# Optimization experiments

Measured on AMD Instinct MI355X. Metric: run time of the kernel, lower is better.

The kernel has to match this reference:

```python
import jax, jax.numpy as jnp
import numpy as np

B, N, K = 8, 2048, 4          # graphs per batch, nodes per graph, knn k
IN_CH, HID, C = 16, 128, 64   # in_channels, GCN hidden, n_clusters
E = 262144                    # input edges


def gcn_conv(x, src, dst, W, b):
    """PyG GCNConv: self-loops + symmetric normalization + linear."""
    n = x.shape[0]
    xw = x @ W
    loop = jnp.arange(n)
    s2 = jnp.concatenate([src, loop])
    d2 = jnp.concatenate([dst, loop])
    deg = jax.ops.segment_sum(jnp.ones(s2.shape[0], x.dtype), d2, num_segments=n)
    dis = jax.lax.rsqrt(deg)  # deg >= 1 thanks to self loops
    norm = dis[s2] * dis[d2]
    return jax.ops.segment_sum(xw[s2] * norm[:, None], d2, num_segments=n) + b


def knn_edges(coords):
    """knn_graph(k=K, loop=False) per graph; edges neighbor->node (source_to_target)."""
    c = coords.reshape(B, N, 3)
    d2 = jnp.sum((c[:, :, None, :] - c[:, None, :, :]) ** 2, -1)  # [B,N,N]
    d2 = d2 + jnp.eye(N, dtype=c.dtype) * jnp.asarray(1e10, c.dtype)  # exclude self
    _, idx = jax.lax.top_k(-d2, K)  # [B,N,K] local neighbor indices
    offs = (jnp.arange(B) * N)[:, None, None]
    src = (idx + offs).reshape(-1)
    dst = (jnp.broadcast_to(jnp.arange(N)[None, :, None], (B, N, K)) + offs).reshape(-1)
    return src, dst


def dmon_pool(x, adj, Wp, bp):
    """PyG DMoNPooling (eval mode, mask all-true since graphs are equal-sized)."""
    s = jax.nn.softmax(x @ Wp + bp, axis=-1)              # [B,N,C]
    out = jax.nn.selu(jnp.einsum('bnc,bnf->bcf', s, x))   # [B,C,F]
    out_adj = jnp.einsum('bnc,bnm,bmd->bcd', s, adj, s)   # [B,C,C]
    deg = adj.sum(1)                                      # column sums, [B,N]
    m = deg.sum(-1) / 2                                   # [B]
    ca = jnp.einsum('bnc,bn->bc', s, deg)                 # [B,C]
    normalizer = ca[:, :, None] * ca[:, None, :] / (2 * m)[:, None, None]
    spectral = (-jnp.trace(out_adj - normalizer, axis1=1, axis2=2) / (2 * m)).mean()
    ss = jnp.einsum('bnc,bnd->bcd', s, s)
    ss_fro = jnp.linalg.norm(ss, axis=(1, 2), keepdims=True)
    i_norm = jnp.sqrt(jnp.asarray(C, x.dtype))            # ||I_C||_F
    i_s = jnp.eye(C, dtype=x.dtype)
    ortho = jnp.linalg.norm(ss / ss_fro - i_s / i_norm, axis=(1, 2)).mean()
    cluster = (jnp.linalg.norm(s.sum(1), axis=1) / N * i_norm - 1).mean()
    return s, out, spectral, ortho, cluster


def forward(x, edge_src, edge_dst, W1, b1, W2, b2, Wp, bp):
    h = jax.nn.relu(gcn_conv(x, edge_src, edge_dst, W1, b1))
    src2, dst2 = knn_edges(h[:, :3])                      # dynamic graph on dims [0,1,2]
    h = jax.nn.relu(gcn_conv(h, src2, dst2, W2, b2))
    xd = h.reshape(B, N, HID)                             # to_dense_batch (equal-size graphs)
    g = edge_src // N                                     # to_dense_adj on ORIGINAL edges
    adj = jnp.zeros((B, N, N), x.dtype).at[g, edge_src % N, edge_dst % N].add(1.0)
    s, out, sp, o, cl = dmon_pool(xd, adj, Wp, bp)
    return jax.nn.log_softmax(out, axis=-1), sp + o + cl, s


def setup_inputs():
    key = jax.random.key(0)
    ks = jax.random.split(key, 8)
    x = jax.random.normal(ks[0], (B * N, IN_CH), jnp.float32)
    g = jax.random.randint(ks[1], (E,), 0, B)
    edge_src = (g * N + jax.random.randint(ks[2], (E,), 0, N)).astype(jnp.int32)
    edge_dst = (g * N + jax.random.randint(ks[3], (E,), 0, N)).astype(jnp.int32)
    batch = jnp.repeat(jnp.arange(B, dtype=jnp.int32), N)
    W1 = jax.random.normal(ks[4], (IN_CH, HID), jnp.float32) / np.sqrt(IN_CH)
    b1 = jnp.zeros((HID,), jnp.float32)
    W2 = jax.random.normal(ks[5], (HID, HID), jnp.float32) / np.sqrt(HID)
    b2 = jnp.zeros((HID,), jnp.float32)
    Wp = jax.random.normal(ks[6], (HID, C), jnp.float32) / np.sqrt(HID)
    bp = jnp.zeros((C,), jnp.float32)
    return {"x": x, "edge_src": edge_src, "edge_dst": edge_dst, "batch": batch,
            "W1": W1, "b1": b1, "W2": W2, "b2": b2, "Wp": Wp, "bp": bp}


def reference(x, edge_src, edge_dst, batch, W1, b1, W2, b2, Wp, bp):
    del batch  # graphs are equal-sized contiguous blocks of N nodes
    return forward(x, edge_src, edge_dst, W1, b1, W2, b2, Wp, bp)
```

## Files before the change

kernel.cpp:

```cpp
#include <hip/hip_runtime.h>
#include <math.h>

#define BGR 8
#define NN 2048
#define KNN 4
#define INCH 16
#define HID 128
#define CL 64
#define NE 262144
#define NT (BGR*NN)

#define OFF_CNT   0
#define OFF_CSR   16384
#define OFF_H1    1064960
#define OFF_NBR   3162112
#define OFF_SS    3227648
#define OFF_H2    4276224
#define OFF_TR    6373376
#define OFF_CA    6373384
#define OFF_SSUM  6373896
#define OFF_MS    6374408
#define OFF_H1C   6374416

__global__ void k_init(int* cnt, float* small, float* loss) {
  int i = blockIdx.x * 256 + threadIdx.x;
  if (i < 16384) cnt[i] = 0;
  int j = i - 16384;
  if (j >= 0 && j < 1040) small[j] = 0.f;
  if (i == 0) loss[0] = 0.f;
}

__global__ void k_bucket(const int* __restrict__ src, const int* __restrict__ dst,
                         int* __restrict__ cnt, int* __restrict__ csr) {
  int e = blockIdx.x * 256 + threadIdx.x;
  if (e >= NE) return;
  int d = dst[e];
  int slot = atomicAdd(&cnt[d], 1);
  if (slot < 64) csr[(d << 6) + slot] = src[e];
}

__global__ __launch_bounds__(256) void k_gemm1(const int* __restrict__ cnt,
    const int* __restrict__ csr, const float* __restrict__ x,
    const float* __restrict__ W1, const float* __restrict__ b1,
    float* __restrict__ h1, float* __restrict__ h1c) {
  __shared__ float a1[16][17];
  __shared__ float w[INCH * HID];
  int tid = threadIdx.x;
  for (int i = tid; i < INCH * HID / 4; i += 256) ((float4*)w)[i] = ((const float4*)W1)[i];
  int nl = tid >> 4, ch = tid & 15;
  int n = blockIdx.x * 16 + nl;
  int cnRaw = cnt[n];
  int cn = cnRaw > 64 ? 64 : cnRaw;
  float dn = rsqrtf((float)cnRaw + 1.0f);
  const int* row = csr + (n << 6);
  float acc = 0.f;
  int sNext = (cn > 0) ? row[0] : 0;
  for (int e = 0; e < cn; e++) {
    int sc = sNext;
    if (e + 1 < cn) sNext = row[e + 1];
    float dis = rsqrtf((float)cnt[sc] + 1.0f);
    acc += x[sc * INCH + ch] * dis;
  }
  a1[nl][ch] = (acc + x[n * INCH + ch] * dn) * dn;
  __syncthreads();
  int j = tid & 127;
  int ng = (tid >> 7) * 8;
#pragma unroll
  for (int u = 0; u < 8; u++) {
    int node = ng + u;
    float s = b1[j];
#pragma unroll
    for (int c2 = 0; c2 < INCH; c2++) s += a1[node][c2] * w[c2 * HID + j];
    float v = fmaxf(s, 0.f);
    h1[(size_t)(blockIdx.x * 16 + node) * HID + j] = v;
    if (j < 4) h1c[(size_t)(blockIdx.x * 16 + node) * 4 + j] = v;
  }
}

__global__ __launch_bounds__(1024) void k_knn(const float* __restrict__ h1c, int* __restrict__ nbr) {
  __shared__ float4 c4[NN];
  int g = blockIdx.y, tid = threadIdx.x;
  const float4* src4 = (const float4*)h1c + (size_t)g * NN;
  for (int i = tid; i < NN; i += 1024) c4[i] = src4[i];
  __syncthreads();
  int wid = tid >> 6, lane = tid & 63;
  int row0 = blockIdx.x * 32 + wid * 2;
  float mx[2], my[2], mz[2];
#pragma unroll
  for (int r = 0; r < 2; r++) { float4 m = c4[row0 + r]; mx[r] = m.x; my[r] = m.y; mz[r] = m.z; }
  unsigned t0[2], t1[2], t2[2], t3[2];
#pragma unroll
  for (int r = 0; r < 2; r++) { t0[r] = t1[r] = t2[r] = t3[r] = 0xFFFFFFFFu; }
#pragma unroll 4
  for (int i = 0; i < 32; i++) {
    int j = i * 64 + lane;
    float4 p = c4[j];
#pragma unroll
    for (int r = 0; r < 2; r++) {
      float dx = p.x - mx[r], dy = p.y - my[r], dz = p.z - mz[r];
      float d2 = dx * dx + dy * dy + dz * dz;
      unsigned k = (__float_as_uint(d2) & 0xFFFFFFE0u) | (unsigned)i;
      if (j == row0 + r) k = 0xFFFFFFFFu;
      unsigned M0 = max(t0[r], k); t0[r] = min(t0[r], k);
      unsigned M1 = max(t1[r], M0); t1[r] = min(t1[r], M0);
      unsigned M2 = max(t2[r], M1); t2[r] = min(t2[r], M1);
      t3[r] = min(t3[r], M2);
    }
  }
#pragma unroll
  for (int r = 0; r < 2; r++) {
    unsigned a0 = t0[r], a1 = t1[r], a2 = t2[r], a3 = t3[r];
    int res[4];
#pragma unroll
    for (int k = 0; k < 4; k++) {
      int cj = (int)((a0 & 31u) << 6) | lane;
      unsigned wd = a0; int wj = cj;
#pragma unroll
      for (int off = 32; off; off >>= 1) {
        unsigned od = (unsigned)__shfl_xor((int)wd, off, 64);
        int oj = __shfl_xor(wj, off, 64);
        bool take = (od < wd) || (od == wd && oj < wj);
        wd = take ? od : wd; wj = take ? oj : wj;
      }
      res[k] = wj;
      bool pop = (cj == wj);
      a0 = pop ? a1 : a0; a1 = pop ? a2 : a1; a2 = pop ? a3 : a2;
      a3 = pop ? 0xFFFFFFFFu : a3;
    }
    if (lane == 0) {
      int node = g * NN + row0 + r;
      ((int4*)nbr)[node] = make_int4(g * NN + res[0], g * NN + res[1],
                                     g * NN + res[2], g * NN + res[3]);
    }
  }
}

__global__ __launch_bounds__(256) void k_gemm2s(const float* __restrict__ h1,
    const int* __restrict__ nbr, const float* __restrict__ W2,
    const float* __restrict__ b2, const float* __restrict__ Wp,
    const float* __restrict__ bp, float* __restrict__ h2,
    float* __restrict__ s_out) {
  __shared__ float smem[6144];
  float (*At)[33] = (float(*)[33])smem;
  float* Bt = smem + 1056;
  float (*H2t)[128] = (float(*)[128])smem;
  float* Wt = smem + 4096;
  int tid = threadIdx.x;
  int rbase = blockIdx.x * 32;
  int r = tid >> 3, q = tid & 7;
  int4 nb = ((const int4*)nbr)[rbase + r];
  const float4* h4 = (const float4*)h1;
  size_t r0 = (size_t)(rbase + r) * 32, rx = (size_t)nb.x * 32, ry = (size_t)nb.y * 32,
         rz = (size_t)nb.z * 32, rw = (size_t)nb.w * 32;
  int rg = tid >> 5;
  int cg = (tid & 31) * 4;
  float acc[4][4];
#pragma unroll
  for (int i = 0; i < 4; i++)
#pragma unroll
    for (int j = 0; j < 4; j++) acc[i][j] = 0.f;
  int kk = tid >> 5;
  int cc = (tid & 31) * 4;
  for (int k0 = 0; k0 < HID; k0 += 32) {
    {
      int q4 = (k0 >> 2) + q;
      float4 a = h4[r0 + q4], bx = h4[rx + q4], by = h4[ry + q4],
             bz = h4[rz + q4], bw = h4[rw + q4];
      int k = q * 4;
      At[r][k]     = (a.x + bx.x + by.x + bz.x + bw.x) * 0.2f;
      At[r][k + 1] = (a.y + bx.y + by.y + bz.y + bw.y) * 0.2f;
      At[r][k + 2] = (a.z + bx.z + by.z + bz.z + bw.z) * 0.2f;
      At[r][k + 3] = (a.w + bx.w + by.w + bz.w + bw.w) * 0.2f;
    }
#pragma unroll
    for (int u = 0; u < 4; u++)
      *(float4*)&Bt[(kk + u * 8) * 128 + cc] = *(const float4*)&W2[(k0 + kk + u * 8) * HID + cc];
    __syncthreads();
#pragma unroll
    for (int k2 = 0; k2 < 32; k2++) {
      float4 bv = *(const float4*)&Bt[k2 * 128 + cg];
#pragma unroll
      for (int i = 0; i < 4; i++) {
        float av = At[rg * 4 + i][k2];
        acc[i][0] += av * bv.x; acc[i][1] += av * bv.y;
        acc[i][2] += av * bv.z; acc[i][3] += av * bv.w;
      }
    }
    __syncthreads();
  }
#pragma unroll
  for (int i = 0; i < 4; i++) {
    int rr = rbase + rg * 4 + i;
#pragma unroll
    for (int j = 0; j < 4; j++) {
      float v = acc[i][j] + b2[cg + j];
      v = fmaxf(v, 0.f);
      h2[(size_t)rr * HID + cg + j] = v;
      H2t[rg * 4 + i][cg + j] = v;
    }
  }
  int c0 = (tid & 31) * 2;
  float acc2[4][2];
  float bp0 = bp[c0], bp1 = bp[c0 + 1];
#pragma unroll
  for (int i = 0; i < 4; i++) { acc2[i][0] = bp0; acc2[i][1] = bp1; }
  for (int kt = 0; kt < 4; kt++) {
    *(float4*)&Wt[tid * 8]     = *(const float4*)&Wp[kt * 2048 + tid * 8];
    *(float4*)&Wt[tid * 8 + 4] = *(const float4*)&Wp[kt * 2048 + tid * 8 + 4];
    __syncthreads();
#pragma unroll
    for (int k2 = 0; k2 < 32; k2++) {
      float w0 = Wt[k2 * 64 + c0];
      float w1 = Wt[k2 * 64 + c0 + 1];
      int kg = kt * 32 + k2;
#pragma unroll
      for (int i = 0; i < 4; i++) {
        float av = H2t[rg * 4 + i][kg];
        acc2[i][0] += av * w0; acc2[i][1] += av * w1;
      }
    }
    __syncthreads();
  }
#pragma unroll
  for (int i = 0; i < 4; i++) {
    float m = fmaxf(acc2[i][0], acc2[i][1]);
    for (int off = 1; off < 32; off <<= 1) m = fmaxf(m, __shfl_xor(m, off, 64));
    float e0 = expf(acc2[i][0] - m), e1 = expf(acc2[i][1] - m);
    float sum = e0 + e1;
    for (int off = 1; off < 32; off <<= 1) sum += __shfl_xor(sum, off, 64);
    float inv = 1.0f / sum;
    size_t o = (size_t)(rbase + rg * 4 + i) * CL + c0;
    s_out[o] = e0 * inv;
    s_out[o + 1] = e1 * inv;
  }
}

__global__ __launch_bounds__(256) void k_dmon_trace(const float* __restrict__ s,
    const float* __restrict__ h2, const int* __restrict__ cnt,
    float* __restrict__ part_pool, float* __restrict__ part_ss,
    float* __restrict__ ca, float* __restrict__ ssum, float* __restrict__ msum,
    const int* __restrict__ src, const int* __restrict__ dst, float* __restrict__ tr) {
  __shared__ float st[64 * 64];
  __shared__ float ht[64 * 128];
  __shared__ float dt[64];
  __shared__ float red[256];
  __shared__ float bins[8];
  int tid = threadIdx.x;
  if (blockIdx.x < 256) {
    int b = blockIdx.x >> 5, sl = blockIdx.x & 31;
    int nb = sl * 64;
    const float* sp = s + ((size_t)b * NN + nb) * CL;
    const float* hp = h2 + ((size_t)b * NN + nb) * HID;
    for (int i = tid; i < 64 * 64 / 4; i += 256) ((float4*)st)[i] = ((const float4*)sp)[i];
    for (int i = tid; i < 64 * 128 / 4; i += 256) ((float4*)ht)[i] = ((const float4*)hp)[i];
    if (tid < 64) dt[tid] = (float)cnt[b * NN + nb + tid];
    __syncthreads();
    int tc = tid & 15, tf = tid >> 4;
    int c0 = tc * 4, f0 = tf * 8;
    float pacc[4][8];
#pragma unroll
    for (int i = 0; i < 4; i++)
#pragma unroll
      for (int j = 0; j < 8; j++) pacc[i][j] = 0.f;
    for (int n = 0; n < 64; n++) {
      float4 sv = *(const float4*)&st[n * 64 + c0];
      float4 ha = *(const float4*)&ht[n * 128 + f0];
      float4 hb = *(const float4*)&ht[n * 128 + f0 + 4];
      float svv[4] = {sv.x, sv.y, sv.z, sv.w};
#pragma unroll
      for (int i = 0; i < 4; i++) {
        pacc[i][0] += svv[i] * ha.x; pacc[i][1] += svv[i] * ha.y;
        pacc[i][2] += svv[i] * ha.z; pacc[i][3] += svv[i] * ha.w;
        pacc[i][4] += svv[i] * hb.x; pacc[i][5] += svv[i] * hb.y;
        pacc[i][6] += svv[i] * hb.z; pacc[i][7] += svv[i] * hb.w;
      }
    }
    float* pp = part_pool + ((size_t)(b * 32 + sl)) * 8192;
#pragma unroll
    for (int i = 0; i < 4; i++) {
      *(float4*)&pp[(c0 + i) * 128 + f0]     = make_float4(pacc[i][0], pacc[i][1], pacc[i][2], pacc[i][3]);
      *(float4*)&pp[(c0 + i) * 128 + f0 + 4] = make_float4(pacc[i][4], pacc[i][5], pacc[i][6], pacc[i][7]);
    }
    int d0 = tf * 4;
    float sacc[4][4];
#pragma unroll
    for (int i = 0; i < 4; i++)
#pragma unroll
      for (int j = 0; j < 4; j++) sacc[i][j] = 0.f;
    for (int n = 0; n < 64; n++) {
      float4 a = *(const float4*)&st[n * 64 + c0];
      float4 bq = *(const float4*)&st[n * 64 + d0];
      float av[4] = {a.x, a.y, a.z, a.w};
#pragma unroll
      for (int i = 0; i < 4; i++) {
        sacc[i][0] += av[i] * bq.x; sacc[i][1] += av[i] * bq.y;
        sacc[i][2] += av[i] * bq.z; sacc[i][3] += av[i] * bq.w;
      }
    }
    float* ps = part_ss + ((size_t)(b * 32 + sl)) * 4096;
#pragma unroll
    for (int i = 0; i < 4; i++)
      *(float4*)&ps[(c0 + i) * 64 + d0] = make_float4(sacc[i][0], sacc[i][1], sacc[i][2], sacc[i][3]);
    int c = tid & 63;
    int q = tid >> 6;
    float a_ss = 0, a_ca = 0, a_m = 0;
    for (int n = q; n < 64; n += 4) {
      float sv = st[n * 64 + c];
      float dv = dt[n];
      a_ss += sv; a_ca += sv * dv;
      if (c == 0) a_m += dv;
    }
    red[tid] = a_ss; __syncthreads();
    if (q == 0) atomicAdd(&ssum[b * CL + c], red[c] + red[64 + c] + red[128 + c] + red[192 + c]);
    __syncthreads();
    red[tid] = a_ca; __syncthreads();
    if (q == 0) atomicAdd(&ca[b * CL + c], red[c] + red[64 + c] + red[128 + c] + red[192 + c]);
    __syncthreads();
    red[tid] = (c == 0) ? a_m : 0.f; __syncthreads();
    if (tid == 0) atomicAdd(&msum[b], red[0] + red[64] + red[128] + red[192]);
  } else {
    if (tid < 8) bins[tid] = 0.f;
    __syncthreads();
    int sub = tid & 15;
    int grp = ((blockIdx.x - 256) * 256 + tid) >> 4;
    const float4* s4 = (const float4*)s;
    for (int e = grp; e < NE; e += 8192) {
      int se = src[e], de = dst[e];
      float4 a = s4[se * 16 + sub];
      float4 b = s4[de * 16 + sub];
      float v = a.x * b.x + a.y * b.y + a.z * b.z + a.w * b.w;
      v += __shfl_xor(v, 1, 64);
      v += __shfl_xor(v, 2, 64);
      v += __shfl_xor(v, 4, 64);
      v += __shfl_xor(v, 8, 64);
      if (sub == 0) atomicAdd(&bins[se >> 11], v);
    }
    __syncthreads();
    if (tid < 8) atomicAdd(&tr[tid], bins[tid]);
  }
}

__global__ __launch_bounds__(256) void k_final(const float* __restrict__ part_pool,
    const float* __restrict__ part_ss, const float* __restrict__ ca,
    const float* __restrict__ ssum, const float* __restrict__ msum,
    const float* __restrict__ tr, float* __restrict__ out, float* __restrict__ outs) {
  int tid = threadIdx.x;
  if (blockIdx.x < 256) {
    __shared__ float r[4], r2[4];
    int half = tid >> 7, f = tid & 127;
    int row = blockIdx.x * 2 + half;
    int wid = tid >> 6;
    const float* p = part_pool + (size_t)(row >> 6) * 32 * 8192 + (row & 63) * 128 + f;
    float v = 0.f;
#pragma unroll
    for (int sl = 0; sl < 32; sl++) v += p[sl * 8192];
    const float scale = 1.0507009873554805f, alpha = 1.6732632423543772f;
    v = scale * (v > 0.f ? v : alpha * expm1f(v));
    float m = v;
    for (int off = 32; off; off >>= 1) m = fmaxf(m, __shfl_xor(m, off, 64));
    if ((tid & 63) == 0) r[wid] = m;
    __syncthreads();
    m = fmaxf(r[half * 2], r[half * 2 + 1]);
    float e = expf(v - m);
    float sum = e;
    for (int off = 32; off; off >>= 1) sum += __shfl_xor(sum, off, 64);
    if ((tid & 63) == 0) r2[wid] = sum;
    __syncthreads();
    sum = r2[half * 2] + r2[half * 2 + 1];
    out[(size_t)row * HID + f] = v - m - logf(sum);
  } else {
    __shared__ float ssb[4096];
    __shared__ float red[256];
    int b = blockIdx.x - 256;
    float loc = 0.f;
    for (int idx = tid; idx < 4096; idx += 256) {
      const float* p = part_ss + (size_t)b * 32 * 4096 + idx;
      float v = 0.f;
#pragma unroll
      for (int sl = 0; sl < 32; sl++) v += p[sl * 4096];
      ssb[idx] = v;
      loc += v * v;
    }
    red[tid] = loc; __syncthreads();
    for (int s2 = 128; s2; s2 >>= 1) { if (tid < s2) red[tid] += red[tid + s2]; __syncthreads(); }
    float fro = sqrtf(red[0]);
    __syncthreads();
    loc = 0.f;
    for (int i = tid; i < 4096; i += 256) {
      float v = ssb[i] / fro - (((i % 65) == 0) ? 0.125f : 0.f);
      loc += v * v;
    }
    red[tid] = loc; __syncthreads();
    for (int s2 = 128; s2; s2 >>= 1) { if (tid < s2) red[tid] += red[tid + s2]; __syncthreads(); }
    float ortho_b = sqrtf(red[0]);
    __syncthreads();
    loc = 0.f;
    if (tid < 64) { float v = ca[b * 64 + tid]; loc = v * v; }
    red[tid] = loc; __syncthreads();
    for (int s2 = 128; s2; s2 >>= 1) { if (tid < s2) red[tid] += red[tid + s2]; __syncthreads(); }
    float caSq = red[0];
    __syncthreads();
    loc = 0.f;
    if (tid < 64) { float v = ssum[b * 64 + tid]; loc = v * v; }
    red[tid] = loc; __syncthreads();
    for (int s2 = 128; s2; s2 >>= 1) { if (tid < s2) red[tid] += red[tid + s2]; __syncthreads(); }
    float ssumSq = red[0];
    __syncthreads();
    if (tid == 0) {
      float m2 = msum[b];
      float spectral_b = -(tr[b] - caSq / m2) / m2;
      float cluster_b = sqrtf(ssumSq) / 2048.0f * 8.0f - 1.0f;
      atomicAdd(&outs[0], (spectral_b + ortho_b + cluster_b) * 0.125f);
    }
  }
}

extern "C" void kernel_launch(void* const* d_in, const int* in_sizes, int n_in,
                              void* d_out, int out_size, void* d_ws, size_t ws_size,
                              hipStream_t stream) {
  (void)in_sizes; (void)n_in; (void)out_size; (void)ws_size;
  const float* x   = (const float*)d_in[0];
  const int* esrc  = (const int*)d_in[1];
  const int* edst  = (const int*)d_in[2];
  const float* W1  = (const float*)d_in[4];
  const float* b1  = (const float*)d_in[5];
  const float* W2  = (const float*)d_in[6];
  const float* b2  = (const float*)d_in[7];
  const float* Wp  = (const float*)d_in[8];
  const float* bp  = (const float*)d_in[9];
  float* out = (float*)d_out;
  float* ws  = (float*)d_ws;

  int*   cnt   = (int*)(ws + OFF_CNT);
  int*   csr   = (int*)(ws + OFF_CSR);
  float* h1    = ws + OFF_H1;
  int*   nbr   = (int*)(ws + OFF_NBR);
  float* h2    = ws + OFF_H2;
  float* tr    = ws + OFF_TR;
  float* ca    = ws + OFF_CA;
  float* ssum  = ws + OFF_SSUM;
  float* msum  = ws + OFF_MS;
  float* h1c   = ws + OFF_H1C;
  float* part_pool = ws + OFF_H1;
  float* part_ss   = ws + OFF_SS;
  float* s_out = out + 65537;

  k_init<<<69, 256, 0, stream>>>(cnt, ws + OFF_TR, out + 65536);
  k_bucket<<<NE / 256, 256, 0, stream>>>(esrc, edst, cnt, csr);
  k_gemm1<<<NT / 16, 256, 0, stream>>>(cnt, csr, x, W1, b1, h1, h1c);
  k_knn<<<dim3(64, 8), 1024, 0, stream>>>(h1c, nbr);
  k_gemm2s<<<NT / 32, 256, 0, stream>>>(h1, nbr, W2, b2, Wp, bp, h2, s_out);
  k_dmon_trace<<<768, 256, 0, stream>>>(s_out, h2, cnt, part_pool, part_ss,
                                        ca, ssum, msum, esrc, edst, tr);
  k_final<<<264, 256, 0, stream>>>(part_pool, part_ss, ca, ssum, msum, tr,
                                   out, out + 65536);
}
```

Baseline: 198.7 us.

## Cache degree norms in LDS, preload Wp during GEMM2, interleave block-to-graph mapping

In gemm1, each block now computes rsqrt degree norms for its whole graph into shared memory once and reuses them, instead of reading cnt per edge inside the gather loop. In gemm2s, all of Wp is staged into a larger shared buffer during the W2 k-loop, so the second projection runs as one loop with no extra barriers. Block indices in gemm2s and dmon_trace are remapped so consecutive blocks fall in different graphs, likely to spread memory traffic across channels. The cost is more LDS per block, which can lower occupancy, plus 2048 redundant rsqrt per gemm1 block.

```diff
diff --git a/kernel.cpp b/kernel.cpp
--- a/kernel.cpp
+++ b/kernel.cpp
@@ -45,21 +45,25 @@
     float* __restrict__ h1, float* __restrict__ h1c) {
   __shared__ float a1[16][17];
   __shared__ float w[INCH * HID];
+  __shared__ float disl[NN];
   int tid = threadIdx.x;
+  int gbase = (blockIdx.x >> 7) * NN;
+  for (int i = tid; i < NN; i += 256)
+    disl[i] = rsqrtf((float)cnt[gbase + i] + 1.0f);
   for (int i = tid; i < INCH * HID / 4; i += 256) ((float4*)w)[i] = ((const float4*)W1)[i];
   int nl = tid >> 4, ch = tid & 15;
   int n = blockIdx.x * 16 + nl;
   int cnRaw = cnt[n];
   int cn = cnRaw > 64 ? 64 : cnRaw;
-  float dn = rsqrtf((float)cnRaw + 1.0f);
   const int* row = csr + (n << 6);
+  __syncthreads();
+  float dn = disl[n - gbase];
   float acc = 0.f;
   int sNext = (cn > 0) ? row[0] : 0;
   for (int e = 0; e < cn; e++) {
     int sc = sNext;
     if (e + 1 < cn) sNext = row[e + 1];
-    float dis = rsqrtf((float)cnt[sc] + 1.0f);
-    acc += x[sc * INCH + ch] * dis;
+    acc += x[sc * INCH + ch] * disl[sc - gbase];
   }
   a1[nl][ch] = (acc + x[n * INCH + ch] * dn) * dn;
   __syncthreads();
@@ -140,13 +144,15 @@
     const float* __restrict__ b2, const float* __restrict__ Wp,
     const float* __restrict__ bp, float* __restrict__ h2,
     float* __restrict__ s_out) {
-  __shared__ float smem[6144];
+  __shared__ float smem[13344];
   float (*At)[33] = (float(*)[33])smem;
   float* Bt = smem + 1056;
   float (*H2t)[128] = (float(*)[128])smem;
-  float* Wt = smem + 4096;
+  float* Wpl = smem + 5152;
   int tid = threadIdx.x;
-  int rbase = blockIdx.x * 32;
+  int bid = blockIdx.x;
+  int rblock = (bid & 7) * 64 + (bid >> 3);
+  int rbase = rblock * 32;
   int r = tid >> 3, q = tid & 7;
   int4 nb = ((const int4*)nbr)[rbase + r];
   const float4* h4 = (const float4*)h1;
@@ -175,6 +181,11 @@
 #pragma unroll
     for (int u = 0; u < 4; u++)
       *(float4*)&Bt[(kk + u * 8) * 128 + cc] = *(const float4*)&W2[(k0 + kk + u * 8) * HID + cc];
+    {
+      int kt = k0 >> 5;
+      *(float4*)&Wpl[kt * 2048 + tid * 8]     = *(const float4*)&Wp[kt * 2048 + tid * 8];
+      *(float4*)&Wpl[kt * 2048 + tid * 8 + 4] = *(const float4*)&Wp[kt * 2048 + tid * 8 + 4];
+    }
     __syncthreads();
 #pragma unroll
     for (int k2 = 0; k2 < 32; k2++) {
@@ -199,27 +210,21 @@
       H2t[rg * 4 + i][cg + j] = v;
     }
   }
+  __syncthreads();
   int c0 = (tid & 31) * 2;
   float acc2[4][2];
   float bp0 = bp[c0], bp1 = bp[c0 + 1];
 #pragma unroll
   for (int i = 0; i < 4; i++) { acc2[i][0] = bp0; acc2[i][1] = bp1; }
-  for (int kt = 0; kt < 4; kt++) {
-    *(float4*)&Wt[tid * 8]     = *(const float4*)&Wp[kt * 2048 + tid * 8];
-    *(float4*)&Wt[tid * 8 + 4] = *(const float4*)&Wp[kt * 2048 + tid * 8 + 4];
-    __syncthreads();
-#pragma unroll
-    for (int k2 = 0; k2 < 32; k2++) {
-      float w0 = Wt[k2 * 64 + c0];
-      float w1 = Wt[k2 * 64 + c0 + 1];
-      int kg = kt * 32 + k2;
-#pragma unroll
-      for (int i = 0; i < 4; i++) {
-        float av = H2t[rg * 4 + i][kg];
-        acc2[i][0] += av * w0; acc2[i][1] += av * w1;
-      }
-    }
-    __syncthreads();
+#pragma unroll 4
+  for (int k2 = 0; k2 < 128; k2++) {
+    float w0 = Wpl[k2 * 64 + c0];
+    float w1 = Wpl[k2 * 64 + c0 + 1];
+#pragma unroll
+    for (int i = 0; i < 4; i++) {
+      float av = H2t[rg * 4 + i][k2];
+      acc2[i][0] += av * w0; acc2[i][1] += av * w1;
+    }
   }
 #pragma unroll
   for (int i = 0; i < 4; i++) {
@@ -247,7 +252,7 @@
   __shared__ float bins[8];
   int tid = threadIdx.x;
   if (blockIdx.x < 256) {
-    int b = blockIdx.x >> 5, sl = blockIdx.x & 31;
+    int b = blockIdx.x & 7, sl = blockIdx.x >> 3;
     int nb = sl * 64;
     const float* sp = s + ((size_t)b * NN + nb) * CL;
     const float* hp = h2 + ((size_t)b * NN + nb) * HID;
```

New measurement: 197.1 us. About the same (-0.8%).
